# Kernel optimization log

Measured on AMD Instinct MI355X. Metric: run time of the kernel, lower is better.

The kernel has to match this reference:

```python
import jax, jax.numpy as jnp
import numpy as np

C_CURV = 0.01   # manifold curvature c
EPS = 1e-7
KH = KW = 3
PAD = 1
STRIDE = 1


def log0(y):
    # Poincare-ball log map at origin: artanh(sqrt(c)||y||) * y / (sqrt(c)||y||)
    sqc = jnp.sqrt(jnp.asarray(C_CURV, y.dtype))
    n = jnp.maximum(jnp.linalg.norm(y, axis=-1, keepdims=True), EPS)
    return jnp.arctanh(jnp.clip(sqc * n, 0.0, 1.0 - 1e-6)) * y / (sqc * n)


def exp0(v):
    # Poincare-ball exp map at origin: tanh(sqrt(c)||v||) * v / (sqrt(c)||v||)
    sqc = jnp.sqrt(jnp.asarray(C_CURV, v.dtype))
    n = jnp.maximum(jnp.linalg.norm(v, axis=-1, keepdims=True), EPS)
    return jnp.tanh(sqc * n) * v / (sqc * n)


def setup_inputs() -> dict:
    key = jax.random.key(0)
    k1, k2, k3 = jax.random.split(key, 3)
    x = jax.random.uniform(k1, (4, 32, 256, 256), dtype=jnp.float32)  # points in ball (c=0.01 -> radius 10)
    Wk = jax.random.normal(k2, (KH * KW, 32, 32), dtype=jnp.float32) * 0.05  # [K, C_out, C_in]
    bias = jax.random.normal(k3, (32,), dtype=jnp.float32) * 0.01
    return {"x": x, "Wk": Wk, "bias": bias}


def reference(x, Wk, bias):
    B, Cin, H, W = x.shape
    Hout = (H + 2 * PAD - KH) // STRIDE + 1
    Wout = (W + 2 * PAD - KW) // STRIDE + 1
    xp = jnp.pad(x, ((0, 0), (0, 0), (PAD, PAD), (PAD, PAD)))
    # unfold: one slice per kernel position (i,j), matching F.unfold's (C_in, K, L) layout
    patches = jnp.stack(
        [xp[:, :, i:i + Hout * STRIDE:STRIDE, j:j + Wout * STRIDE:STRIDE]
         for i in range(KH) for j in range(KW)], axis=0)      # [K, B, Cin, Hout, Wout]
    u = log0(jnp.moveaxis(patches, 2, -1))                    # [K, B, Hout, Wout, Cin] tangent vectors
    # PVFC (mobius matvec = exp0(W @ log0(x))) followed by log0 cancels the exp0:
    # log0(PVFC_k(x)) = W_k @ log0(x). Aggregate (sum over k) fused into the einsum.
    v = jnp.einsum('kbhwc,koc->bhwo', u, Wk)                  # [B, Hout, Wout, Cout]
    v = jax.nn.relu(v + bias)
    out = exp0(v)                                             # back to manifold
    return jnp.transpose(out, (0, 3, 1, 2))                   # [B, Cout, Hout, Wout]
```

## Files before the change

### kernel.cpp

```cpp
#include <hip/hip_runtime.h>
#include <math.h>


#define TW 32
#define TH 8
#define HW_ 34
#define NPIX 340
#define CIN 32
#define COUT 32
#define U_BYTES 21760
#define W_ROWS 288

typedef __attribute__((ext_vector_type(8))) short bf16x8;
typedef __attribute__((ext_vector_type(4))) float f32x4;

__device__ inline unsigned short f2bf(float f) {
    unsigned int u = __builtin_bit_cast(unsigned int, f);
    unsigned int r = (u + 0x7FFFu + ((u >> 16) & 1u)) >> 16;
    return (unsigned short)r;
}

__global__ __launch_bounds__(256, 4) void pvconv_kernel(
    const float* __restrict__ x, const float* __restrict__ Wk,
    const float* __restrict__ bias, float* __restrict__ out)
{
    __shared__ __align__(16) unsigned char smem[U_BYTES + W_ROWS * 64];
    unsigned char* u8 = smem;
    unsigned char* w8 = smem + U_BYTES;
    float*         v  = (float*)smem;

    const int t  = threadIdx.x;
    const int bx = blockIdx.x, by = blockIdx.y, b = blockIdx.z;
    const int x0 = bx * TW, y0 = by * TH;

    for (int f = t; f < W_ROWS * 4; f += 256) {
        int r = f >> 2, j = f & 3;
        const float4* src = (const float4*)(Wk + r * 32 + j * 8);
        float4 a = src[0], c = src[1];
        unsigned int pk[4];
        pk[0] = (unsigned int)f2bf(a.x) | ((unsigned int)f2bf(a.y) << 16);
        pk[1] = (unsigned int)f2bf(a.z) | ((unsigned int)f2bf(a.w) << 16);
        pk[2] = (unsigned int)f2bf(c.x) | ((unsigned int)f2bf(c.y) << 16);
        pk[3] = (unsigned int)f2bf(c.z) | ((unsigned int)f2bf(c.w) << 16);
        int sw = j ^ ((r >> 1) & 3);
        *(uint4*)(w8 + r * 64 + sw * 16) = *(uint4*)pk;
    }

    for (int p = t; p < NPIX; p += 256) {
        int py = p / HW_, px = p - py * HW_;
        int gy = y0 - 1 + py, gx = x0 - 1 + px;
        float vv[CIN];
        if ((unsigned)gy < 256u && (unsigned)gx < 256u) {
            const float* xp = x + (size_t)b * CIN * 65536 + gy * 256 + gx;
            #pragma unroll
            for (int c = 0; c < CIN; ++c) vv[c] = xp[(size_t)c * 65536];
        } else {
            #pragma unroll
            for (int c = 0; c < CIN; ++c) vv[c] = 0.f;
        }
        float ss = 0.f;
        #pragma unroll
        for (int c = 0; c < CIN; ++c) ss = fmaf(vv[c], vv[c], ss);
        float n = fmaxf(sqrtf(ss), 1e-7f);
        float z = fminf(0.1f * n, 1.f - 1e-6f);
        float at = 0.5f * __logf((1.f + z) / (1.f - z));
        float s = at / (0.1f * n);
        int swb = (p >> 1) & 3;
        uint4* row = (uint4*)(u8 + p * 64);
        #pragma unroll
        for (int j = 0; j < 4; ++j) {
            unsigned int pk[4];
            #pragma unroll
            for (int w = 0; w < 4; ++w)
                pk[w] = (unsigned int)f2bf(vv[j * 8 + 2 * w] * s)
                      | ((unsigned int)f2bf(vv[j * 8 + 2 * w + 1] * s) << 16);
            row[j ^ swb] = *(uint4*)pk;
        }
    }
    __syncthreads();

    const int wv = t >> 6, lane = t & 63;
    const int m = lane & 15, quad = lane >> 4;

    f32x4 acc[2][4];
    #pragma unroll
    for (int n = 0; n < 2; ++n)
        #pragma unroll
        for (int mt = 0; mt < 4; ++mt) acc[n][mt] = (f32x4)0.f;

    int apix[4];
    #pragma unroll
    for (int mt = 0; mt < 4; ++mt) {
        int pb = wv * 64 + mt * 16;
        apix[mt] = (pb >> 5) * HW_ + (pb & 31) + m;
    }

    #pragma unroll
    for (int tap = 0; tap < 9; ++tap) {
        const int dy = tap / 3, dx = tap - dy * 3;
        const int hoff = dy * HW_ + dx;
        int r0 = tap * 32 + m;
        int swB = quad ^ ((r0 >> 1) & 3);
        bf16x8 bf0 = *(const bf16x8*)(w8 + r0 * 64 + swB * 16);
        bf16x8 bf1 = *(const bf16x8*)(w8 + (r0 + 16) * 64 + swB * 16);
        #pragma unroll
        for (int mt = 0; mt < 4; ++mt) {
            int hp = apix[mt] + hoff;
            bf16x8 af = *(const bf16x8*)(u8 + hp * 64 + ((quad ^ ((hp >> 1) & 3)) << 4));
            acc[0][mt] = __builtin_amdgcn_mfma_f32_16x16x32_bf16(af, bf0, acc[0][mt], 0, 0, 0);
            acc[1][mt] = __builtin_amdgcn_mfma_f32_16x16x32_bf16(af, bf1, acc[1][mt], 0, 0, 0);
        }
    }

    const float bia0 = bias[m], bia1 = bias[16 + m];
    __syncthreads();

    #pragma unroll
    for (int n = 0; n < 2; ++n)
        #pragma unroll
        for (int mt = 0; mt < 4; ++mt)
            #pragma unroll
            for (int r = 0; r < 4; ++r) {
                int pix = wv * 64 + mt * 16 + quad * 4 + r;
                float val = acc[n][mt][r] + (n ? bia1 : bia0);
                v[pix * 36 + n * 16 + m] = fmaxf(val, 0.f);
            }
    __syncthreads();

    {
        float q[COUT];
        const float4* vp = (const float4*)(smem + (size_t)t * 144);
        #pragma unroll
        for (int j = 0; j < 8; ++j) {
            float4 c4 = vp[j];
            q[4 * j] = c4.x; q[4 * j + 1] = c4.y; q[4 * j + 2] = c4.z; q[4 * j + 3] = c4.w;
        }
        float ss = 0.f;
        #pragma unroll
        for (int o = 0; o < COUT; ++o) ss = fmaf(q[o], q[o], ss);
        float n = fmaxf(sqrtf(ss), 1e-7f);
        float a = 0.1f * n;
        float e = __expf(-2.f * a);
        float s = (1.f - e) / ((1.f + e) * a);
        const int px = t & 31, py = t >> 5;
        const size_t base = (size_t)b * COUT * 65536 + (size_t)(y0 + py) * 256 + (x0 + px);
        #pragma unroll
        for (int o = 0; o < COUT; ++o)
            out[base + (size_t)o * 65536] = s * q[o];
    }
}

extern "C" void kernel_launch(void* const* d_in, const int* in_sizes, int n_in,
                              void* d_out, int out_size, void* d_ws, size_t ws_size,
                              hipStream_t stream) {
    const float* x    = (const float*)d_in[0];
    const float* Wk   = (const float*)d_in[1];
    const float* bias = (const float*)d_in[2];
    float* out = (float*)d_out;

    dim3 grid(256 / TW, 256 / TH, 4);
    dim3 block(256);
    pvconv_kernel<<<grid, block, 0, stream>>>(x, Wk, bias, out);
}
```

Before: 98.00 us.

## Overlap halo staging with MFMA, prep bf16 weights in separate kernel, bf16 epilogue

Moves the weight fp32-to-bf16 conversion into a small pre-kernel that writes to the workspace, and the main kernel reads B fragments straight from global memory instead of staging them in LDS. Input staging is split in two: the first 204 pixels are staged, then waves 0-1 run their MFMAs while waves 2-3 stage the remaining halo pixels, after which waves 2-3 run their MFMAs. The pre-exp0 activations are stored to LDS as bf16 in a channel-major transposed layout, and output uses nontemporal stores. This cuts LDS footprint and serial staging time, but adds a second launch, rounds the post-ReLU values to bf16 before the norm, and reads weights from global memory inside the MFMA loop.

```diff
diff --git a/kernel.cpp b/kernel.cpp
--- a/kernel.cpp
+++ b/kernel.cpp
@@ -8,136 +8,137 @@
 #define NPIX 340
 #define CIN 32
 #define COUT 32
-#define U_BYTES 21760
-#define W_ROWS 288
+#define VSTR 258
 
 typedef __attribute__((ext_vector_type(8))) short bf16x8;
 typedef __attribute__((ext_vector_type(4))) float f32x4;
 
 __device__ inline unsigned short f2bf(float f) {
     unsigned int u = __builtin_bit_cast(unsigned int, f);
-    unsigned int r = (u + 0x7FFFu + ((u >> 16) & 1u)) >> 16;
-    return (unsigned short)r;
+    return (unsigned short)((u + 0x7FFFu + ((u >> 16) & 1u)) >> 16);
+}
+__device__ inline unsigned int pk2(float a, float b) {
+    return (unsigned int)f2bf(a) | ((unsigned int)f2bf(b) << 16);
+}
+
+__global__ __launch_bounds__(256) void wprep_kernel(
+    const float* __restrict__ Wk, unsigned short* __restrict__ wsW)
+{
+    int i = blockIdx.x * 256 + threadIdx.x;
+    if (i < 9 * 32 * 32) wsW[i] = f2bf(Wk[i]);
+}
+
+__device__ inline void stage_pixel(int p, int x0, int y0, int b,
+                                   const float* __restrict__ x,
+                                   unsigned char* __restrict__ u8)
+{
+    int py = p / HW_, px = p - py * HW_;
+    int gy = y0 - 1 + py, gx = x0 - 1 + px;
+    float vv[CIN];
+    if ((unsigned)gy < 256u && (unsigned)gx < 256u) {
+        const float* xp = x + (size_t)b * CIN * 65536 + gy * 256 + gx;
+        #pragma unroll
+        for (int c = 0; c < CIN; ++c) vv[c] = xp[(size_t)c * 65536];
+    } else {
+        #pragma unroll
+        for (int c = 0; c < CIN; ++c) vv[c] = 0.f;
+    }
+    float ss = 0.f;
+    #pragma unroll
+    for (int c = 0; c < CIN; ++c) ss = fmaf(vv[c], vv[c], ss);
+    float n = fmaxf(sqrtf(ss), 1e-7f);
+    float z = fminf(0.1f * n, 1.f - 1e-6f);
+    float at = 0.5f * __logf((1.f + z) / (1.f - z));
+    float s = at / (0.1f * n);
+    int swb = (p >> 1) & 3;
+    uint4* row = (uint4*)(u8 + p * 64);
+    #pragma unroll
+    for (int j = 0; j < 4; ++j) {
+        unsigned int pk[4];
+        #pragma unroll
+        for (int w = 0; w < 4; ++w)
+            pk[w] = pk2(vv[j * 8 + 2 * w] * s, vv[j * 8 + 2 * w + 1] * s);
+        row[j ^ swb] = *(uint4*)pk;
+    }
 }
 
 __global__ __launch_bounds__(256, 4) void pvconv_kernel(
-    const float* __restrict__ x, const float* __restrict__ Wk,
+    const float* __restrict__ x, const unsigned short* __restrict__ wsW,
     const float* __restrict__ bias, float* __restrict__ out)
 {
-    __shared__ __align__(16) unsigned char smem[U_BYTES + W_ROWS * 64];
-    unsigned char* u8 = smem;
-    unsigned char* w8 = smem + U_BYTES;
-    float*         v  = (float*)smem;
+    __shared__ __align__(16) unsigned char smem[21760 + COUT * VSTR * 2];
+    unsigned char*  u8 = smem;
+    unsigned short* v  = (unsigned short*)(smem + 21760);
 
     const int t  = threadIdx.x;
-    const int bx = blockIdx.x, by = blockIdx.y, b = blockIdx.z;
-    const int x0 = bx * TW, y0 = by * TH;
+    const int x0 = blockIdx.x * TW, y0 = blockIdx.y * TH, b = blockIdx.z;
+    const int wv = t >> 6, lane = t & 63, m = lane & 15, quad = lane >> 4;
 
-    for (int f = t; f < W_ROWS * 4; f += 256) {
-        int r = f >> 2, j = f & 3;
-        const float4* src = (const float4*)(Wk + r * 32 + j * 8);
-        float4 a = src[0], c = src[1];
-        unsigned int pk[4];
-        pk[0] = (unsigned int)f2bf(a.x) | ((unsigned int)f2bf(a.y) << 16);
-        pk[1] = (unsigned int)f2bf(a.z) | ((unsigned int)f2bf(a.w) << 16);
-        pk[2] = (unsigned int)f2bf(c.x) | ((unsigned int)f2bf(c.y) << 16);
-        pk[3] = (unsigned int)f2bf(c.z) | ((unsigned int)f2bf(c.w) << 16);
-        int sw = j ^ ((r >> 1) & 3);
-        *(uint4*)(w8 + r * 64 + sw * 16) = *(uint4*)pk;
-    }
+    if (t < 204) stage_pixel(t, x0, y0, b, x, u8);
+    __syncthreads();
 
-    for (int p = t; p < NPIX; p += 256) {
-        int py = p / HW_, px = p - py * HW_;
-        int gy = y0 - 1 + py, gx = x0 - 1 + px;
-        float vv[CIN];
-        if ((unsigned)gy < 256u && (unsigned)gx < 256u) {
-            const float* xp = x + (size_t)b * CIN * 65536 + gy * 256 + gx;
+    auto do_mfma = [&]() {
+        f32x4 acc[2][4];
+        #pragma unroll
+        for (int n = 0; n < 2; ++n)
             #pragma unroll
-            for (int c = 0; c < CIN; ++c) vv[c] = xp[(size_t)c * 65536];
-        } else {
+            for (int mt = 0; mt < 4; ++mt) acc[n][mt] = (f32x4)0.f;
+
+        int apix[4];
+        #pragma unroll
+        for (int mt = 0; mt < 4; ++mt) {
+            int pb = wv * 64 + mt * 16;
+            apix[mt] = (pb >> 5) * HW_ + (pb & 31) + m;
+        }
+        #pragma unroll
+        for (int tap = 0; tap < 9; ++tap) {
+            const int dy = tap / 3, dx = tap - 3 * dy;
+            const int hoff = dy * HW_ + dx;
+            const unsigned short* wrow = wsW + (tap * 32 + m) * 32 + quad * 8;
+            bf16x8 B0 = *(const bf16x8*)wrow;
+            bf16x8 B1 = *(const bf16x8*)(wrow + 512);
             #pragma unroll
-            for (int c = 0; c < CIN; ++c) vv[c] = 0.f;
+            for (int mt = 0; mt < 4; ++mt) {
+                int hp = apix[mt] + hoff;
+                bf16x8 A = *(const bf16x8*)(u8 + hp * 64 + ((quad ^ ((hp >> 1) & 3)) << 4));
+                acc[0][mt] = __builtin_amdgcn_mfma_f32_16x16x32_bf16(A, B0, acc[0][mt], 0, 0, 0);
+                acc[1][mt] = __builtin_amdgcn_mfma_f32_16x16x32_bf16(A, B1, acc[1][mt], 0, 0, 0);
+            }
         }
-        float ss = 0.f;
+        const float bia0 = bias[m], bia1 = bias[16 + m];
         #pragma unroll
-        for (int c = 0; c < CIN; ++c) ss = fmaf(vv[c], vv[c], ss);
-        float n = fmaxf(sqrtf(ss), 1e-7f);
-        float z = fminf(0.1f * n, 1.f - 1e-6f);
-        float at = 0.5f * __logf((1.f + z) / (1.f - z));
-        float s = at / (0.1f * n);
-        int swb = (p >> 1) & 3;
-        uint4* row = (uint4*)(u8 + p * 64);
-        #pragma unroll
-        for (int j = 0; j < 4; ++j) {
-            unsigned int pk[4];
+        for (int n = 0; n < 2; ++n)
             #pragma unroll
-            for (int w = 0; w < 4; ++w)
-                pk[w] = (unsigned int)f2bf(vv[j * 8 + 2 * w] * s)
-                      | ((unsigned int)f2bf(vv[j * 8 + 2 * w + 1] * s) << 16);
-            row[j ^ swb] = *(uint4*)pk;
-        }
+            for (int mt = 0; mt < 4; ++mt)
+                #pragma unroll
+                for (int r = 0; r < 4; ++r) {
+                    int pix = wv * 64 + mt * 16 + quad * 4 + r;
+                    float val = acc[n][mt][r] + (n ? bia1 : bia0);
+                    v[(n * 16 + m) * VSTR + pix] = f2bf(fmaxf(val, 0.f));
+                }
+    };
+
+    if (wv < 2) {
+        do_mfma();
+    } else {
+        int t2 = t - 128;
+        stage_pixel(204 + t2, x0, y0, b, x, u8);
+        if (t2 < 8) stage_pixel(332 + t2, x0, y0, b, x, u8);
     }
     __syncthreads();
 
-    const int wv = t >> 6, lane = t & 63;
-    const int m = lane & 15, quad = lane >> 4;
-
-    f32x4 acc[2][4];
-    #pragma unroll
-    for (int n = 0; n < 2; ++n)
-        #pragma unroll
-        for (int mt = 0; mt < 4; ++mt) acc[n][mt] = (f32x4)0.f;
-
-    int apix[4];
-    #pragma unroll
-    for (int mt = 0; mt < 4; ++mt) {
-        int pb = wv * 64 + mt * 16;
-        apix[mt] = (pb >> 5) * HW_ + (pb & 31) + m;
-    }
-
-    #pragma unroll
-    for (int tap = 0; tap < 9; ++tap) {
-        const int dy = tap / 3, dx = tap - dy * 3;
-        const int hoff = dy * HW_ + dx;
-        int r0 = tap * 32 + m;
-        int swB = quad ^ ((r0 >> 1) & 3);
-        bf16x8 bf0 = *(const bf16x8*)(w8 + r0 * 64 + swB * 16);
-        bf16x8 bf1 = *(const bf16x8*)(w8 + (r0 + 16) * 64 + swB * 16);
-        #pragma unroll
-        for (int mt = 0; mt < 4; ++mt) {
-            int hp = apix[mt] + hoff;
-            bf16x8 af = *(const bf16x8*)(u8 + hp * 64 + ((quad ^ ((hp >> 1) & 3)) << 4));
-            acc[0][mt] = __builtin_amdgcn_mfma_f32_16x16x32_bf16(af, bf0, acc[0][mt], 0, 0, 0);
-            acc[1][mt] = __builtin_amdgcn_mfma_f32_16x16x32_bf16(af, bf1, acc[1][mt], 0, 0, 0);
-        }
-    }
-
-    const float bia0 = bias[m], bia1 = bias[16 + m];
-    __syncthreads();
-
-    #pragma unroll
-    for (int n = 0; n < 2; ++n)
-        #pragma unroll
-        for (int mt = 0; mt < 4; ++mt)
-            #pragma unroll
-            for (int r = 0; r < 4; ++r) {
-                int pix = wv * 64 + mt * 16 + quad * 4 + r;
-                float val = acc[n][mt][r] + (n ? bia1 : bia0);
-                v[pix * 36 + n * 16 + m] = fmaxf(val, 0.f);
-            }
+    if (wv >= 2) do_mfma();
     __syncthreads();
 
     {
         float q[COUT];
-        const float4* vp = (const float4*)(smem + (size_t)t * 144);
-        #pragma unroll
-        for (int j = 0; j < 8; ++j) {
-            float4 c4 = vp[j];
-            q[4 * j] = c4.x; q[4 * j + 1] = c4.y; q[4 * j + 2] = c4.z; q[4 * j + 3] = c4.w;
-        }
         float ss = 0.f;
         #pragma unroll
-        for (int o = 0; o < COUT; ++o) ss = fmaf(q[o], q[o], ss);
+        for (int o = 0; o < COUT; ++o) {
+            unsigned int w16 = v[o * VSTR + t];
+            q[o] = __builtin_bit_cast(float, w16 << 16);
+            ss = fmaf(q[o], q[o], ss);
+        }
         float n = fmaxf(sqrtf(ss), 1e-7f);
         float a = 0.1f * n;
         float e = __expf(-2.f * a);
@@ -146,7 +147,7 @@
         const size_t base = (size_t)b * COUT * 65536 + (size_t)(y0 + py) * 256 + (x0 + px);
         #pragma unroll
         for (int o = 0; o < COUT; ++o)
-            out[base + (size_t)o * 65536] = s * q[o];
+            __builtin_nontemporal_store(s * q[o], &out[base + (size_t)o * 65536]);
     }
 }
 
@@ -157,8 +158,9 @@
     const float* Wk   = (const float*)d_in[1];
     const float* bias = (const float*)d_in[2];
     float* out = (float*)d_out;
+    unsigned short* wsW = (unsigned short*)d_ws;
 
+    wprep_kernel<<<dim3(36), dim3(256), 0, stream>>>(Wk, wsW);
     dim3 grid(256 / TW, 256 / TH, 4);
-    dim3 block(256);
-    pvconv_kernel<<<grid, block, 0, stream>>>(x, Wk, bias, out);
+    pvconv_kernel<<<grid, dim3(256), 0, stream>>>(x, wsW, bias, out);
 }
```

Measured after the change: 99.73 us. No clear change (+1.8%).
